# Optimization experiments

Hardware: AMD Instinct MI355X
Metric: run time of the kernel (lower is better)

Reference implementation:

```python
import jax, jax.numpy as jnp
import numpy as np

LAMBDA_SOFTMAX = 9.0
LAMBDA_LSE = 6.0
EPS = 1e-8
LEAKY_SLOPE = 0.1


def setup_inputs() -> dict:
    key = jax.random.key(0)
    k1, k2, k3, k4 = jax.random.split(key, 4)
    B, R, L, D = 256, 36, 40, 1024  # n_image=n_caption=B, n_regions, max_words, embed
    return {
        'pool_img': jax.random.normal(k1, (B, D), jnp.float32),
        'img_emb': jax.random.normal(k2, (B, R, D), jnp.float32),
        'pool_txt': jax.random.normal(k3, (B, D), jnp.float32),
        'cap_emb': jax.random.normal(k4, (B, L, D), jnp.float32),
    }


def _l2norm(x, axis):
    return x / (jnp.sqrt(jnp.sum(x * x, axis=axis, keepdims=True)) + EPS)


def _lse_reduce(m):
    # mul_(lambda_lse).exp_() ; sum over singleton dim ; log / lambda_lse
    return jnp.log(jnp.exp(m * LAMBDA_LSE)) / LAMBDA_LSE


def _text_score_one(cap_i, txt_poo_i, images):
    # cap_i: (L, d) query; images: (B, R, d) context. clipped_l2norm variant.
    attn = jnp.einsum('brd,ld->brl', images, cap_i)            # (B, R, L)
    attn = jax.nn.leaky_relu(attn, LEAKY_SLOPE)
    attn = _l2norm(attn, axis=2)                               # l2norm over queryL
    attn = jnp.swapaxes(attn, 1, 2)                            # (B, L, R)
    attn = jax.nn.softmax(attn * LAMBDA_SOFTMAX, axis=-1)      # softmax over regions
    wctx = jnp.einsum('blr,brd->bld', attn, images)            # (B, L, d)
    w12 = jnp.einsum('bld,d->bl', wctx, txt_poo_i)
    w1 = jnp.sqrt(jnp.sum(txt_poo_i * txt_poo_i))
    w2 = jnp.sqrt(jnp.sum(wctx * wctx, axis=2))
    sim = w12 / jnp.maximum(w1 * w2, EPS)                      # (B, L)
    return _lse_reduce(jnp.mean(sim, axis=1))                  # (B,)


def _image_score_one(cap_i, img_emb, img_poo):
    # query: img_emb (B, R, d); context: cap_i (L, d) broadcast over B.
    attn = jnp.einsum('ld,brd->blr', cap_i, img_emb)           # (B, L, R)
    attn = jax.nn.leaky_relu(attn, LEAKY_SLOPE)
    attn = _l2norm(attn, axis=2)                               # l2norm over regions
    attn = jnp.swapaxes(attn, 1, 2)                            # (B, R, L)
    attn = jax.nn.softmax(attn * LAMBDA_SOFTMAX, axis=-1)      # softmax over words
    wctx = jnp.einsum('brl,ld->brd', attn, cap_i)              # (B, R, d)
    w12 = jnp.einsum('brd,bd->br', wctx, img_poo)
    w1 = jnp.sqrt(jnp.sum(img_poo * img_poo, axis=1, keepdims=True))  # (B,1)
    w2 = jnp.sqrt(jnp.sum(wctx * wctx, axis=2))                # (B, R)
    sim = w12 / jnp.maximum(w1 * w2, EPS)
    return _lse_reduce(jnp.mean(sim, axis=1))                  # (B,)


def reference(pool_img, img_emb, pool_txt, cap_emb):
    # scores_t2i: loop over captions -> vmap; result (n_cap, n_image) -> transpose
    t2i = jax.vmap(_text_score_one, in_axes=(0, 0, None))(cap_emb, pool_txt, img_emb).T
    i2t = jax.vmap(_image_score_one, in_axes=(0, None, None))(cap_emb, img_emb, pool_img).T
    base = pool_img @ pool_txt.T
    return t2i + i2t + base
```

## Files before the change

### kernel.cpp

```cpp
#include <hip/hip_runtime.h>

typedef unsigned short u16;
typedef __attribute__((ext_vector_type(8))) short bf16x8;
typedef __attribute__((ext_vector_type(4))) float f32x4;

#define D_EMB 1024
#define NBAT  256
#define AS1 __attribute__((address_space(1)))
#define AS3 __attribute__((address_space(3)))

__device__ __forceinline__ u16 f2bf(float f){
    unsigned int u = __float_as_uint(f);
    unsigned int r = (u + 0x7fffu + ((u >> 16) & 1u)) >> 16;
    return (u16)r;
}
__device__ __forceinline__ float leaky(float x){ return x > 0.f ? x : 0.1f * x; }

__global__ void pack_kernel(const float* __restrict__ pool_img, const float* __restrict__ img_emb,
                            const float* __restrict__ pool_txt, const float* __restrict__ cap_emb,
                            u16* __restrict__ imgw, u16* __restrict__ capw){
    int row = blockIdx.x;
    const float* src; u16* dst;
    if (row < NBAT * 37){
        int e = row / 37, rr = row - e * 37;
        src = (rr < 36) ? (img_emb + ((size_t)e * 36 + rr) * D_EMB) : (pool_img + (size_t)e * D_EMB);
        dst = imgw + (size_t)row * D_EMB;
    } else {
        int r2 = row - NBAT * 37;
        int e = r2 / 41, rr = r2 - e * 41;
        src = (rr < 40) ? (cap_emb + ((size_t)e * 40 + rr) * D_EMB) : (pool_txt + (size_t)e * D_EMB);
        dst = capw + (size_t)r2 * D_EMB;
    }
    int t = threadIdx.x;
    float4 v = ((const float4*)src)[t];
    unsigned long long pk = (unsigned long long)f2bf(v.x)
        | ((unsigned long long)f2bf(v.y) << 16)
        | ((unsigned long long)f2bf(v.z) << 32)
        | ((unsigned long long)f2bf(v.w) << 48);
    *(unsigned long long*)(dst + (size_t)t * 4) = pk;
}

__global__ void norm_kernel(const float* __restrict__ pool_img, const float* __restrict__ pool_txt,
                            float* __restrict__ w1i, float* __restrict__ w1t){
    __shared__ float red[256];
    int v = blockIdx.x;
    const float* src = (v < 256) ? (pool_img + (size_t)v * D_EMB)
                                 : (pool_txt + (size_t)(v - 256) * D_EMB);
    int t = threadIdx.x;
    float4 x = ((const float4*)src)[t];
    red[t] = x.x*x.x + x.y*x.y + x.z*x.z + x.w*x.w;
    __syncthreads();
    for (int off = 128; off > 0; off >>= 1){
        if (t < off) red[t] += red[t + off];
        __syncthreads();
    }
    if (t == 0){
        float n = sqrtf(red[0]);
        if (v < 256) w1i[v] = n; else w1t[v - 256] = n;
    }
}

__launch_bounds__(256, 2)
__global__ void gram_kernel(const u16* __restrict__ imgw, const u16* __restrict__ capw,
                            float* __restrict__ G, float* __restrict__ H){
    __shared__ __align__(16) char gsm[6144];
    int blk = blockIdx.x;
    int tid = threadIdx.x, lane = tid & 63;
    int wave = __builtin_amdgcn_readfirstlane(tid >> 6);
    int frow = lane & 15, q = lane >> 4;

    const u16* E; float* Gout; int R;
    if (blk < NBAT){ E = imgw + (size_t)blk * 37 * D_EMB; Gout = G + (size_t)blk * 1296; R = 36; }
    else { int b = blk - NBAT; E = capw + (size_t)b * 41 * D_EMB; Gout = H + (size_t)b * 1600; R = 40; }

    {
        uint4 z = {0u,0u,0u,0u};
        for (int off = tid * 16; off < 6144; off += 4096) *(uint4*)(gsm + off) = z;
    }

    const u16* gsrc[2]; int goff[2]; bool gval[2];
    #pragma unroll
    for (int j = 0; j < 2; ++j){
        int g = wave + j * 4;
        gval[j] = false; gsrc[j] = E; goff[j] = 0;
        if (g < 6){
            int kk = g / 3, t = g - kk * 3;
            int row = t * 16 + frow;
            gsrc[j] = E + (size_t)row * D_EMB + kk * 32 + q * 8;
            goff[j] = g * 1024;
            gval[j] = (row < R);
        }
    }

    int wm = wave >> 1, wn = wave & 1;
    int nTm = wm ? 1 : 2, nTn = wn ? 1 : 2;
    f32x4 acc[2][2];
    #pragma unroll
    for (int a = 0; a < 2; ++a)
        #pragma unroll
        for (int b = 0; b < 2; ++b) acc[a][b] = (f32x4){0.f,0.f,0.f,0.f};

    for (int c = 0; c < 16; ++c){
        __syncthreads();
        #pragma unroll
        for (int j = 0; j < 2; ++j){
            if (gval[j]){
                __builtin_amdgcn_global_load_lds(
                    (const AS1 void*)(const void*)(gsrc[j] + c * 64),
                    (AS3 void*)(void*)(gsm + goff[j] + lane * 16),
                    16, 0, 0);
            }
        }
        __syncthreads();
        #pragma unroll
        for (int kk = 0; kk < 2; ++kk){
            bf16x8 fA[2], fB[2];
            #pragma unroll
            for (int mi = 0; mi < 2; ++mi)
                if (mi < nTm) fA[mi] = *(const bf16x8*)(gsm + ((kk * 3 + (wm + mi * 2)) * 64 + lane) * 16);
            #pragma unroll
            for (int ni = 0; ni < 2; ++ni)
                if (ni < nTn) fB[ni] = *(const bf16x8*)(gsm + ((kk * 3 + (wn + ni * 2)) * 64 + lane) * 16);
            #pragma unroll
            for (int mi = 0; mi < 2; ++mi)
                if (mi < nTm)
                    #pragma unroll
                    for (int ni = 0; ni < 2; ++ni)
                        if (ni < nTn)
                            acc[mi][ni] = __builtin_amdgcn_mfma_f32_16x16x32_bf16(
                                fA[mi], fB[ni], acc[mi][ni], 0, 0, 0);
        }
    }

    #pragma unroll
    for (int mi = 0; mi < 2; ++mi){
        if (mi < nTm){
            int tm = wm + mi * 2;
            #pragma unroll
            for (int ni = 0; ni < 2; ++ni){
                if (ni < nTn){
                    int tn = wn + ni * 2;
                    int col = tn * 16 + frow;
                    if (col < R){
                        #pragma unroll
                        for (int g = 0; g < 4; ++g){
                            int row = tm * 16 + q * 4 + g;
                            if (row < R) Gout[row * R + col] = acc[mi][ni][g];
                        }
                    }
                }
            }
        }
    }
}

__launch_bounds__(256, 5)
__global__ void fused_kernel(const u16* __restrict__ imgw, const u16* __restrict__ capw,
                             const float* __restrict__ G, const float* __restrict__ H,
                             const float* __restrict__ w1i, const float* __restrict__ w1t,
                             float* __restrict__ out){
    __shared__ __align__(16) char smem[26624];
    float* Call = (float*)smem;
    float* rnb  = (float*)(smem + 25160);
    float* cnb  = (float*)(smem + 25736);

    int tid  = threadIdx.x;
    int lane = tid & 63;
    int wave = __builtin_amdgcn_readfirstlane(tid >> 6);
    int frow = lane & 15, q = lane >> 4;

    int lin = blockIdx.x;
    int pan = lin >> 10;
    int rem = lin & 1023;
    int b_t = rem >> 3;
    int i_t = (pan << 3) | (rem & 7);
    int b0 = b_t * 2, i0 = i_t * 2;
    const u16* Ag = imgw + (size_t)b0 * 37 * D_EMB;
    const u16* Bg = capw + (size_t)i0 * 41 * D_EMB;

    {
        uint4 z = {0u,0u,0u,0u};
        for (int off = tid * 16; off < 22528; off += 4096) *(uint4*)(smem + off) = z;
    }

    const u16* gsrc[6]; int goff[6]; bool gval[6];
    #pragma unroll
    for (int j = 0; j < 6; ++j){
        int g = wave + j * 4;
        gval[j] = false; gsrc[j] = Ag; goff[j] = 0;
        if (g < 22){
            if (g < 10){
                int tm = g % 5, kk = g / 5;
                int row = tm * 16 + frow;
                gsrc[j] = Ag + (size_t)row * D_EMB + kk * 32 + q * 8;
                goff[j] = g * 1024;
                gval[j] = (row < 74);
            } else {
                int gb = g - 10;
                int tn = gb % 6, kk = gb / 6;
                int row = tn * 16 + frow;
                gsrc[j] = Bg + (size_t)row * D_EMB + kk * 32 + q * 8;
                goff[j] = 10240 + gb * 1024;
                gval[j] = (row < 82);
            }
        }
    }

    int wm = wave >> 1, wn = wave & 1;
    int nTm = wm ? 2 : 3;
    f32x4 acc[3][3];
    #pragma unroll
    for (int aa = 0; aa < 3; ++aa)
        #pragma unroll
        for (int bb = 0; bb < 3; ++bb) acc[aa][bb] = (f32x4){0.f, 0.f, 0.f, 0.f};

    for (int c = 0; c < 16; ++c){
        __syncthreads();
        #pragma unroll
        for (int j = 0; j < 6; ++j){
            if (gval[j]){
                __builtin_amdgcn_global_load_lds(
                    (const AS1 void*)(const void*)(gsrc[j] + c * 64),
                    (AS3 void*)(void*)(smem + goff[j] + lane * 16),
                    16, 0, 0);
            }
        }
        __syncthreads();
        #pragma unroll
        for (int kk = 0; kk < 2; ++kk){
            bf16x8 bfr[3];
            #pragma unroll
            for (int ni = 0; ni < 3; ++ni){
                int tn = wn + ni * 2;
                bfr[ni] = *(const bf16x8*)(smem + 10240 + ((kk * 6 + tn) * 64 + lane) * 16);
            }
            #pragma unroll
            for (int mi = 0; mi < 3; ++mi){
                if (mi < nTm){
                    int tm = wm + mi * 2;
                    bf16x8 af = *(const bf16x8*)(smem + ((kk * 5 + tm) * 64 + lane) * 16);
                    #pragma unroll
                    for (int ni = 0; ni < 3; ++ni){
                        acc[mi][ni] = __builtin_amdgcn_mfma_f32_16x16x32_bf16(
                            af, bfr[ni], acc[mi][ni], 0, 0, 0);
                    }
                }
            }
        }
    }
    __syncthreads();

    #pragma unroll
    for (int mi = 0; mi < 3; ++mi){
        if (mi < nTm){
            int tm = wm + mi * 2;
            #pragma unroll
            for (int ni = 0; ni < 3; ++ni){
                int tn = wn + ni * 2;
                int col = tn * 16 + frow;
                int rbase = tm * 16 + q * 4;
                if (col < 82){
                    #pragma unroll
                    for (int g = 0; g < 4; ++g){
                        int rowc = rbase + g;
                        if (rowc < 74) Call[rowc * 85 + col] = acc[mi][ni][g];
                    }
                }
            }
        }
    }
    __syncthreads();

    int pb = wave >> 1, pi = wave & 1;
    int bg = b0 + pb, ig = i0 + pi;
    const float* Sv = Call + (pb * 37) * 85 + pi * 41;
    const float* Gb = G + (size_t)bg * 1296;
    const float* Hi = H + (size_t)ig * 1600;
    float w1_txt = w1t[ig];
    float w1_img = w1i[bg];

    {
        int r0 = (lane < 36) ? lane : 35;
        float s = 0.f;
        #pragma unroll
        for (int l = 0; l < 40; ++l){ float x = leaky(Sv[r0 * 85 + l]); s = fmaf(x, x, s); }
        if (lane < 36) rnb[wave * 36 + lane] = 1.f / (sqrtf(s) + 1e-8f);
    }
    float t2i_sum;
    {
        int lc = (lane < 40) ? lane : 39;
        float u[36], dd = 0.f, num = 0.f;
        #pragma unroll
        for (int r = 0; r < 36; ++r){
            float x = leaky(Sv[r * 85 + lc]);
            float e = __expf(9.0f * x * rnb[wave * 36 + r]);
            u[r] = e; dd += e;
            num = fmaf(e, Sv[r * 85 + 40], num);
        }
        float zz = 0.f;
        #pragma unroll
        for (int rr = 0; rr < 36; ++rr){
            float t = 0.f;
            #pragma unroll
            for (int r2 = rr + 1; r2 < 36; ++r2) t = fmaf(Gb[rr * 36 + r2], u[r2], t);
            zz += (2.f * t + Gb[rr * 36 + rr] * u[rr]) * u[rr];
        }
        float w2s = sqrtf(fmaxf(zz, 0.f));
        float sim = (num / dd) / fmaxf(w1_txt * w2s / dd, 1e-8f);
        sim = (lane < 40) ? sim : 0.f;
        #pragma unroll
        for (int off = 32; off > 0; off >>= 1) sim += __shfl_down(sim, off);
        t2i_sum = sim;
    }

    {
        int l0 = (lane < 40) ? lane : 39;
        float s = 0.f;
        #pragma unroll
        for (int r = 0; r < 36; ++r){ float x = leaky(Sv[r * 85 + l0]); s = fmaf(x, x, s); }
        if (lane < 40) cnb[wave * 40 + lane] = 1.f / (sqrtf(s) + 1e-8f);
    }
    float i2t_sum;
    {
        int rc = (lane < 36) ? lane : 35;
        float v[40], dd = 0.f, num = 0.f;
        #pragma unroll
        for (int l = 0; l < 40; ++l){
            float x = leaky(Sv[rc * 85 + l]);
            float e = __expf(9.0f * x * cnb[wave * 40 + l]);
            v[l] = e; dd += e;
            num = fmaf(e, Sv[36 * 85 + l], num);
        }
        float zz = 0.f;
        #pragma unroll
        for (int ll = 0; ll < 40; ++ll){
            float t = 0.f;
            #pragma unroll
            for (int l2 = ll + 1; l2 < 40; ++l2) t = fmaf(Hi[ll * 40 + l2], v[l2], t);
            zz += (2.f * t + Hi[ll * 40 + ll] * v[ll]) * v[ll];
        }
        float w2s = sqrtf(fmaxf(zz, 0.f));
        float sim = (num / dd) / fmaxf(w1_img * w2s / dd, 1e-8f);
        sim = (lane < 36) ? sim : 0.f;
        #pragma unroll
        for (int off = 32; off > 0; off >>= 1) sim += __shfl_down(sim, off);
        i2t_sum = sim;
    }

    if (lane == 0)
        out[bg * 256 + ig] = t2i_sum * (1.f / 40.f) + i2t_sum * (1.f / 36.f) + Sv[36 * 85 + 40];
}

extern "C" void kernel_launch(void* const* d_in, const int* in_sizes, int n_in,
                              void* d_out, int out_size, void* d_ws, size_t ws_size,
                              hipStream_t stream){
    const float* pool_img = (const float*)d_in[0];
    const float* img_emb  = (const float*)d_in[1];
    const float* pool_txt = (const float*)d_in[2];
    const float* cap_emb  = (const float*)d_in[3];
    float* out = (float*)d_out;

    char* ws = (char*)d_ws;
    size_t o = 0;
    u16* imgw = (u16*)(ws + o);  o += (size_t)256 * 37 * 1024 * 2;
    u16* capw = (u16*)(ws + o);  o += (size_t)256 * 41 * 1024 * 2;
    float* G  = (float*)(ws + o); o += (size_t)256 * 36 * 36 * 4;
    float* H  = (float*)(ws + o); o += (size_t)256 * 40 * 40 * 4;
    float* w1i = (float*)(ws + o); o += 1024;
    float* w1t = (float*)(ws + o); o += 1024;

    pack_kernel<<<19968, 256, 0, stream>>>(pool_img, img_emb, pool_txt, cap_emb, imgw, capw);
    norm_kernel<<<512, 256, 0, stream>>>(pool_img, pool_txt, w1i, w1t);
    gram_kernel<<<512, 256, 0, stream>>>(imgw, capw, G, H);
    fused_kernel<<<16384, 256, 0, stream>>>(imgw, capw, G, H, w1i, w1t, out);
}
```

Baseline: 867.2 us.

## Pack softmax weights as bf16 pairs, remap blocks per XCD, simplify sim

The per-lane exponentials used in the Gram quadratic form are stored as truncated bf16 pairs packed into 32-bit registers, roughly halving the register arrays (36/40 floats down to 18/20 words). The aim is lower VGPR pressure, which helps meet the 5-waves launch bound without spilling. The block index mapping is also changed so each XCD (blockIdx mod 8) covers a contiguous range of image tiles, improving L2 reuse. The sim formula cancels the common dd factor, and w1 loads move to the point of use. The bf16 truncation adds rounding error to the quadratic form, and extra unpack instructions are added in the inner loops.

```diff
diff --git a/kernel.cpp b/kernel.cpp
--- a/kernel.cpp
+++ b/kernel.cpp
@@ -15,6 +15,12 @@
     return (u16)r;
 }
 __device__ __forceinline__ float leaky(float x){ return x > 0.f ? x : 0.1f * x; }
+
+__device__ __forceinline__ unsigned pack2(float a, float b){
+    return (__float_as_uint(a) >> 16) | (__float_as_uint(b) & 0xffff0000u);
+}
+__device__ __forceinline__ float unpk_lo(unsigned p){ return __uint_as_float(p << 16); }
+__device__ __forceinline__ float unpk_hi(unsigned p){ return __uint_as_float(p & 0xffff0000u); }
 
 __global__ void pack_kernel(const float* __restrict__ pool_img, const float* __restrict__ img_emb,
                             const float* __restrict__ pool_txt, const float* __restrict__ cap_emb,
@@ -170,10 +176,10 @@
     int frow = lane & 15, q = lane >> 4;
 
     int lin = blockIdx.x;
-    int pan = lin >> 10;
-    int rem = lin & 1023;
-    int b_t = rem >> 3;
-    int i_t = (pan << 3) | (rem & 7);
+    int xcd = lin & 7;
+    int s   = lin >> 3;
+    int b_t = (xcd << 4) | (s & 15);
+    int i_t = s >> 4;
     int b0 = b_t * 2, i0 = i_t * 2;
     const u16* Ag = imgw + (size_t)b0 * 37 * D_EMB;
     const u16* Bg = capw + (size_t)i0 * 41 * D_EMB;
@@ -276,37 +282,43 @@
     const float* Sv = Call + (pb * 37) * 85 + pi * 41;
     const float* Gb = G + (size_t)bg * 1296;
     const float* Hi = H + (size_t)ig * 1600;
-    float w1_txt = w1t[ig];
-    float w1_img = w1i[bg];
 
     {
         int r0 = (lane < 36) ? lane : 35;
-        float s = 0.f;
-        #pragma unroll
-        for (int l = 0; l < 40; ++l){ float x = leaky(Sv[r0 * 85 + l]); s = fmaf(x, x, s); }
-        if (lane < 36) rnb[wave * 36 + lane] = 1.f / (sqrtf(s) + 1e-8f);
+        float s2 = 0.f;
+        #pragma unroll
+        for (int l = 0; l < 40; ++l){ float x = leaky(Sv[r0 * 85 + l]); s2 = fmaf(x, x, s2); }
+        if (lane < 36) rnb[wave * 36 + lane] = 1.f / (sqrtf(s2) + 1e-8f);
     }
     float t2i_sum;
     {
         int lc = (lane < 40) ? lane : 39;
-        float u[36], dd = 0.f, num = 0.f;
-        #pragma unroll
-        for (int r = 0; r < 36; ++r){
-            float x = leaky(Sv[r * 85 + lc]);
-            float e = __expf(9.0f * x * rnb[wave * 36 + r]);
-            u[r] = e; dd += e;
-            num = fmaf(e, Sv[r * 85 + 40], num);
+        unsigned up[18];
+        float dd = 0.f, num = 0.f;
+        #pragma unroll
+        for (int r = 0; r < 36; r += 2){
+            float x0 = leaky(Sv[r * 85 + lc]);
+            float e0 = __expf(9.0f * x0 * rnb[wave * 36 + r]);
+            float x1 = leaky(Sv[(r + 1) * 85 + lc]);
+            float e1 = __expf(9.0f * x1 * rnb[wave * 36 + r + 1]);
+            dd += e0 + e1;
+            num = fmaf(e0, Sv[r * 85 + 40], fmaf(e1, Sv[(r + 1) * 85 + 40], num));
+            up[r >> 1] = pack2(e0, e1);
         }
         float zz = 0.f;
         #pragma unroll
         for (int rr = 0; rr < 36; ++rr){
+            float urr = (rr & 1) ? unpk_hi(up[rr >> 1]) : unpk_lo(up[rr >> 1]);
             float t = 0.f;
             #pragma unroll
-            for (int r2 = rr + 1; r2 < 36; ++r2) t = fmaf(Gb[rr * 36 + r2], u[r2], t);
-            zz += (2.f * t + Gb[rr * 36 + rr] * u[rr]) * u[rr];
+            for (int r2 = rr + 1; r2 < 36; ++r2){
+                float ur2 = (r2 & 1) ? unpk_hi(up[r2 >> 1]) : unpk_lo(up[r2 >> 1]);
+                t = fmaf(Gb[rr * 36 + r2], ur2, t);
+            }
+            zz += (2.f * t + Gb[rr * 36 + rr] * urr) * urr;
         }
         float w2s = sqrtf(fmaxf(zz, 0.f));
-        float sim = (num / dd) / fmaxf(w1_txt * w2s / dd, 1e-8f);
+        float sim = num / fmaxf(w1t[ig] * w2s, 1e-8f);
         sim = (lane < 40) ? sim : 0.f;
         #pragma unroll
         for (int off = 32; off > 0; off >>= 1) sim += __shfl_down(sim, off);
@@ -315,32 +327,40 @@
 
     {
         int l0 = (lane < 40) ? lane : 39;
-        float s = 0.f;
-        #pragma unroll
-        for (int r = 0; r < 36; ++r){ float x = leaky(Sv[r * 85 + l0]); s = fmaf(x, x, s); }
-        if (lane < 40) cnb[wave * 40 + lane] = 1.f / (sqrtf(s) + 1e-8f);
+        float s2 = 0.f;
+        #pragma unroll
+        for (int r = 0; r < 36; ++r){ float x = leaky(Sv[r * 85 + l0]); s2 = fmaf(x, x, s2); }
+        if (lane < 40) cnb[wave * 40 + lane] = 1.f / (sqrtf(s2) + 1e-8f);
     }
     float i2t_sum;
     {
         int rc = (lane < 36) ? lane : 35;
-        float v[40], dd = 0.f, num = 0.f;
-        #pragma unroll
-        for (int l = 0; l < 40; ++l){
-            float x = leaky(Sv[rc * 85 + l]);
-            float e = __expf(9.0f * x * cnb[wave * 40 + l]);
-            v[l] = e; dd += e;
-            num = fmaf(e, Sv[36 * 85 + l], num);
+        unsigned vp[20];
+        float dd = 0.f, num = 0.f;
+        #pragma unroll
+        for (int l = 0; l < 40; l += 2){
+            float x0 = leaky(Sv[rc * 85 + l]);
+            float e0 = __expf(9.0f * x0 * cnb[wave * 40 + l]);
+            float x1 = leaky(Sv[rc * 85 + l + 1]);
+            float e1 = __expf(9.0f * x1 * cnb[wave * 40 + l + 1]);
+            dd += e0 + e1;
+            num = fmaf(e0, Sv[36 * 85 + l], fmaf(e1, Sv[36 * 85 + l + 1], num));
+            vp[l >> 1] = pack2(e0, e1);
         }
         float zz = 0.f;
         #pragma unroll
         for (int ll = 0; ll < 40; ++ll){
+            float vll = (ll & 1) ? unpk_hi(vp[ll >> 1]) : unpk_lo(vp[ll >> 1]);
             float t = 0.f;
             #pragma unroll
-            for (int l2 = ll + 1; l2 < 40; ++l2) t = fmaf(Hi[ll * 40 + l2], v[l2], t);
-            zz += (2.f * t + Hi[ll * 40 + ll] * v[ll]) * v[ll];
+            for (int l2 = ll + 1; l2 < 40; ++l2){
+                float vl2 = (l2 & 1) ? unpk_hi(vp[l2 >> 1]) : unpk_lo(vp[l2 >> 1]);
+                t = fmaf(Hi[ll * 40 + l2], vl2, t);
+            }
+            zz += (2.f * t + Hi[ll * 40 + ll] * vll) * vll;
         }
         float w2s = sqrtf(fmaxf(zz, 0.f));
-        float sim = (num / dd) / fmaxf(w1_img * w2s / dd, 1e-8f);
+        float sim = num / fmaxf(w1i[bg] * w2s, 1e-8f);
         sim = (lane < 36) ? sim : 0.f;
         #pragma unroll
         for (int off = 32; off > 0; off >>= 1) sim += __shfl_down(sim, off);
```

Result: faster. 753.4 us (-13.1%).
